# Optimization experiments

Measured on AMD Instinct MI355X. Metric: run time of the kernel, lower is better.

## Reference

```python
import jax, jax.numpy as jnp
import numpy as np
import math

H = 16
D_MODEL = 1024
D_K = 64
BS = 8
SEQ = 1024


def setup_inputs() -> dict:
    key = jax.random.key(0)
    ks = jax.random.split(key, 13)
    s = 1.0 / math.sqrt(D_MODEL)
    inp = {
        "q": jax.random.normal(ks[0], (BS, SEQ, D_MODEL), dtype=jnp.float32),
        "k": jax.random.normal(ks[1], (BS, SEQ, D_MODEL), dtype=jnp.float32),
        "v": jax.random.normal(ks[2], (BS, SEQ, D_MODEL), dtype=jnp.float32),
        "mask": jax.random.randint(ks[3], (BS, SEQ, SEQ), 0, 2, dtype=jnp.int32),
        "Wq": jax.random.normal(ks[4], (D_MODEL, D_MODEL), dtype=jnp.float32) * s,
        "bq": jax.random.normal(ks[5], (D_MODEL,), dtype=jnp.float32) * s,
        "Wk": jax.random.normal(ks[6], (D_MODEL, D_MODEL), dtype=jnp.float32) * s,
        "bk": jax.random.normal(ks[7], (D_MODEL,), dtype=jnp.float32) * s,
        "Wv": jax.random.normal(ks[8], (D_MODEL, D_MODEL), dtype=jnp.float32) * s,
        "bv": jax.random.normal(ks[9], (D_MODEL,), dtype=jnp.float32) * s,
        "Wo": jax.random.normal(ks[10], (D_MODEL, D_MODEL), dtype=jnp.float32) * s,
        "bo": jax.random.normal(ks[11], (D_MODEL,), dtype=jnp.float32) * s,
    }
    return inp


def reference(q, k, v, mask, Wq, bq, Wk, bk, Wv, bv, Wo, bo):
    bs, seq, _ = q.shape
    # projections, split heads: [b, h, s, dk]
    def proj(x, W, b):
        y = x @ W + b
        return y.reshape(bs, seq, H, D_K).transpose(0, 2, 1, 3)
    qh = proj(q, Wq, bq)
    kh = proj(k, Wk, bk)
    vh = proj(v, Wv, bv)
    # scaled dot-product attention (dropout is identity in eval mode)
    scores = jnp.einsum("bhqd,bhkd->bhqk", qh, kh) / math.sqrt(D_K)
    scores = jnp.where(mask[:, None, :, :] == 0, jnp.float32(-1e9), scores)
    attn = jax.nn.softmax(scores, axis=-1)
    ctx = jnp.einsum("bhqk,bhkd->bhqd", attn, vh)
    concat = ctx.transpose(0, 2, 1, 3).reshape(bs, seq, D_MODEL)
    return concat @ Wo + bo
```

## Files before the change

### kernel.cpp

```cpp
#include <hip/hip_runtime.h>
#include <hip/hip_bf16.h>
#include <math.h>

#define HN 16
#define DM 1024
#define DK 64
#define BSZ 8
#define SEQL 1024

typedef __attribute__((ext_vector_type(8))) short bf16x8;
typedef __attribute__((ext_vector_type(4))) short short4v;
typedef __attribute__((ext_vector_type(4))) float f32x4;

__device__ __forceinline__ short f2bf(float f) {
    union { float f; unsigned u; } x; x.f = f;
    unsigned u = x.u + 0x7FFFu + ((x.u >> 16) & 1u);
    return (short)(u >> 16);
}

__global__ __launch_bounds__(256) void transpose_cast(const float* __restrict__ W,
                                                      short* __restrict__ Wt) {
    __shared__ float tile[32][33];
    const int t = threadIdx.x;
    const int k0 = blockIdx.x * 32, n0 = blockIdx.y * 32;
    const int c = t & 31, r = t >> 5;
    #pragma unroll
    for (int p = 0; p < 4; ++p)
        tile[r + 8 * p][c] = W[(size_t)(k0 + r + 8 * p) * DM + n0 + c];
    __syncthreads();
    #pragma unroll
    for (int p = 0; p < 4; ++p)
        Wt[(size_t)(n0 + r + 8 * p) * DM + k0 + c] = f2bf(tile[c][r + 8 * p]);
}

template <int MODE>
__global__ __launch_bounds__(256) void gemm_mfma(const void* __restrict__ Ap,
                                                 const short* __restrict__ Wt,
                                                 const float* __restrict__ bias,
                                                 void* __restrict__ Cp) {
    __shared__ __attribute__((aligned(16))) short As[128][40];
    __shared__ __attribute__((aligned(16))) short Bs[128][40];
    const int t = threadIdx.x;
    const int lane = t & 63, wv = t >> 6;
    const int wm = (wv >> 1) * 64, wn = (wv & 1) * 64;
    const int quad = lane >> 4, l15 = lane & 15;
    const int tileM = blockIdx.x * 128, tileN = blockIdx.y * 128;
    const size_t zoff = (size_t)blockIdx.z * DM * SEQL;

    f32x4 acc[4][4];
    #pragma unroll
    for (int i = 0; i < 4; ++i)
        #pragma unroll
        for (int j = 0; j < 4; ++j) acc[i][j] = {0.f, 0.f, 0.f, 0.f};

    for (int k0 = 0; k0 < DM; k0 += 32) {
        if (MODE == 0) {
            const float* A = (const float*)Ap + zoff;
            const int r0 = t >> 3, c4 = (t & 7) * 4;
            #pragma unroll
            for (int p = 0; p < 4; ++p) {
                int row = r0 + 32 * p;
                float4 v = *(const float4*)(A + (size_t)(tileM + row) * DM + k0 + c4);
                short4v s4 = {f2bf(v.x), f2bf(v.y), f2bf(v.z), f2bf(v.w)};
                *(short4v*)&As[row][c4] = s4;
            }
        } else {
            const short* A = (const short*)Ap + zoff;
            const int r0 = t >> 2, c8 = (t & 3) * 8;
            #pragma unroll
            for (int p = 0; p < 2; ++p) {
                int row = r0 + 64 * p;
                *(bf16x8*)&As[row][c8] =
                    *(const bf16x8*)(A + (size_t)(tileM + row) * DM + k0 + c8);
            }
        }
        {
            const int r0 = t >> 2, c8 = (t & 3) * 8;
            #pragma unroll
            for (int p = 0; p < 2; ++p) {
                int row = r0 + 64 * p;
                *(bf16x8*)&Bs[row][c8] =
                    *(const bf16x8*)(Wt + (size_t)(tileN + row) * DM + k0 + c8);
            }
        }
        __syncthreads();
        bf16x8 a[4], b[4];
        #pragma unroll
        for (int i = 0; i < 4; ++i) a[i] = *(const bf16x8*)&As[wm + i * 16 + l15][quad * 8];
        #pragma unroll
        for (int j = 0; j < 4; ++j) b[j] = *(const bf16x8*)&Bs[wn + j * 16 + l15][quad * 8];
        #pragma unroll
        for (int i = 0; i < 4; ++i)
            #pragma unroll
            for (int j = 0; j < 4; ++j)
                acc[i][j] = __builtin_amdgcn_mfma_f32_16x16x32_bf16(a[i], b[j], acc[i][j], 0, 0, 0);
        __syncthreads();
    }

    #pragma unroll
    for (int i = 0; i < 4; ++i)
        #pragma unroll
        for (int j = 0; j < 4; ++j)
            #pragma unroll
            for (int rr = 0; rr < 4; ++rr) {
                int row = tileM + wm + i * 16 + quad * 4 + rr;
                int col = tileN + wn + j * 16 + l15;
                float v = acc[i][j][rr] + bias[col];
                if (MODE == 0) {
                    short* C = (short*)Cp + zoff;
                    C[((size_t)(col >> 6) * SEQL + row) * DK + (col & 63)] = f2bf(v);
                } else {
                    float* C = (float*)Cp + zoff;
                    C[(size_t)row * DM + col] = v;
                }
            }
}

__global__ __launch_bounds__(256) void attn_mfma(const short* __restrict__ Qw,
                                                 const short* __restrict__ Kw,
                                                 const short* __restrict__ Vw,
                                                 const int* __restrict__ mask,
                                                 short* __restrict__ ctx) {
    __shared__ __attribute__((aligned(16))) short Qs[64][72];
    __shared__ __attribute__((aligned(16))) short Ks[64][72];
    __shared__ __attribute__((aligned(16))) short Vs[64][72];
    __shared__ __attribute__((aligned(16))) short Ps[4][16][72];
    const int t = threadIdx.x;
    const int lane = t & 63, w = t >> 6;
    const int quad = lane >> 4, l15 = lane & 15;
    const int q0 = blockIdx.x * 64;
    const int h = blockIdx.y;
    const size_t zoff = (size_t)blockIdx.z * DM * SEQL;
    const short* Qb = Qw + zoff + (size_t)h * SEQL * DK;
    const short* Kb = Kw + zoff + (size_t)h * SEQL * DK;
    const short* Vb = Vw + zoff + (size_t)h * SEQL * DK;
    const int* mb = mask + (size_t)blockIdx.z * SEQL * SEQL;

    #pragma unroll
    for (int p = 0; p < 2; ++p) {
        int cc = t + 256 * p;
        int row = cc >> 3, off = (cc & 7) * 8;
        *(bf16x8*)&Qs[row][off] = *(const bf16x8*)(Qb + (size_t)(q0 + row) * DK + off);
    }

    f32x4 o[4];
    #pragma unroll
    for (int td = 0; td < 4; ++td) o[td] = {0.f, 0.f, 0.f, 0.f};
    float Lacc[4] = {0.f, 0.f, 0.f, 0.f};

    for (int j0 = 0; j0 < SEQL; j0 += 64) {
        #pragma unroll
        for (int p = 0; p < 2; ++p) {
            int cc = t + 256 * p;
            int row = cc >> 3, off = (cc & 7) * 8;
            *(bf16x8*)&Ks[row][off] = *(const bf16x8*)(Kb + (size_t)(j0 + row) * DK + off);
        }
        {
            int r = t >> 2, c16 = (t & 3) * 16;
            bf16x8 v0 = *(const bf16x8*)(Vb + (size_t)(j0 + r) * DK + c16);
            bf16x8 v1 = *(const bf16x8*)(Vb + (size_t)(j0 + r) * DK + c16 + 8);
            #pragma unroll
            for (int u = 0; u < 8; ++u) Vs[c16 + u][r] = v0[u];
            #pragma unroll
            for (int u = 0; u < 8; ++u) Vs[c16 + 8 + u][r] = v1[u];
        }
        __syncthreads();

        #pragma unroll
        for (int tn = 0; tn < 4; ++tn) {
            f32x4 s = {0.f, 0.f, 0.f, 0.f};
            #pragma unroll
            for (int ks = 0; ks < 2; ++ks) {
                bf16x8 aq = *(const bf16x8*)&Qs[w * 16 + l15][ks * 32 + quad * 8];
                bf16x8 bk = *(const bf16x8*)&Ks[tn * 16 + l15][ks * 32 + quad * 8];
                s = __builtin_amdgcn_mfma_f32_16x16x32_bf16(aq, bk, s, 0, 0, 0);
            }
            #pragma unroll
            for (int rr = 0; rr < 4; ++rr) {
                int rq = q0 + w * 16 + quad * 4 + rr;
                int cj = j0 + tn * 16 + l15;
                float p = mb[(size_t)rq * SEQL + cj] ? __expf(s[rr] * 0.125f) : 0.0f;
                Lacc[rr] += p;
                Ps[w][quad * 4 + rr][tn * 16 + l15] = f2bf(p);
            }
        }
        __syncthreads();

        #pragma unroll
        for (int td = 0; td < 4; ++td)
            #pragma unroll
            for (int ks = 0; ks < 2; ++ks) {
                bf16x8 ap = *(const bf16x8*)&Ps[w][l15][ks * 32 + quad * 8];
                bf16x8 bv = *(const bf16x8*)&Vs[td * 16 + l15][ks * 32 + quad * 8];
                o[td] = __builtin_amdgcn_mfma_f32_16x16x32_bf16(ap, bv, o[td], 0, 0, 0);
            }
        __syncthreads();
    }

    #pragma unroll
    for (int rr = 0; rr < 4; ++rr) {
        float l = Lacc[rr];
        l += __shfl_xor(l, 1);
        l += __shfl_xor(l, 2);
        l += __shfl_xor(l, 4);
        l += __shfl_xor(l, 8);
        Lacc[rr] = 1.0f / l;
    }
    short* cb = ctx + zoff;
    #pragma unroll
    for (int td = 0; td < 4; ++td)
        #pragma unroll
        for (int rr = 0; rr < 4; ++rr) {
            int rq = q0 + w * 16 + quad * 4 + rr;
            int cd = h * 64 + td * 16 + l15;
            cb[(size_t)rq * DM + cd] = f2bf(o[td][rr] * Lacc[rr]);
        }
}

extern "C" void kernel_launch(void* const* d_in, const int* in_sizes, int n_in,
                              void* d_out, int out_size, void* d_ws, size_t ws_size,
                              hipStream_t stream) {
    const float* q  = (const float*)d_in[0];
    const float* k  = (const float*)d_in[1];
    const float* v  = (const float*)d_in[2];
    const int* mask = (const int*)d_in[3];
    const float* Wq = (const float*)d_in[4];
    const float* bq = (const float*)d_in[5];
    const float* Wk = (const float*)d_in[6];
    const float* bk = (const float*)d_in[7];
    const float* Wv = (const float*)d_in[8];
    const float* bv = (const float*)d_in[9];
    const float* Wo = (const float*)d_in[10];
    const float* bo = (const float*)d_in[11];
    float* out = (float*)d_out;

    const size_t MEL = (size_t)1024 * 1024;
    short* wsb = (short*)d_ws;
    short* Wqt = wsb;
    short* Wkt = wsb + MEL;
    short* Wvt = wsb + 2 * MEL;
    short* Wot = wsb + 3 * MEL;

    transpose_cast<<<dim3(32, 32), 256, 0, stream>>>(Wq, Wqt);
    transpose_cast<<<dim3(32, 32), 256, 0, stream>>>(Wk, Wkt);
    transpose_cast<<<dim3(32, 32), 256, 0, stream>>>(Wv, Wvt);
    transpose_cast<<<dim3(32, 32), 256, 0, stream>>>(Wo, Wot);

    const bool full = ws_size >= ((size_t)80 << 20);
    const int zdim = full ? BSZ : 1;
    const int iters = full ? 1 : BSZ;

    const size_t bufEl = full ? 8 * MEL : MEL;
    short* Qw  = wsb + 4 * MEL;
    short* Kw  = Qw + bufEl;
    short* Vw  = Kw + bufEl;
    short* ctx = Vw + bufEl;

    for (int it = 0; it < iters; ++it) {
        const float* qb = q + (size_t)it * MEL;
        const float* kb = k + (size_t)it * MEL;
        const float* vb = v + (size_t)it * MEL;
        const int* mbp  = mask + (size_t)it * MEL;
        float* ob       = out + (size_t)it * MEL;

        gemm_mfma<0><<<dim3(8, 8, zdim), 256, 0, stream>>>(qb, Wqt, bq, Qw);
        gemm_mfma<0><<<dim3(8, 8, zdim), 256, 0, stream>>>(kb, Wkt, bk, Kw);
        gemm_mfma<0><<<dim3(8, 8, zdim), 256, 0, stream>>>(vb, Wvt, bv, Vw);

        attn_mfma<<<dim3(16, 16, zdim), 256, 0, stream>>>(Qw, Kw, Vw, mbp, ctx);

        gemm_mfma<1><<<dim3(8, 8, zdim), 256, 0, stream>>>(ctx, Wot, bo, ob);
    }
}
```

Baseline: 440.8 us.

## Restructure MHA pipeline: bit-packed mask, fused QKV launch, register-resident attention

```diff
diff --git a/kernel.cpp b/kernel.cpp
--- a/kernel.cpp
+++ b/kernel.cpp
@@ -1,6 +1,5 @@
 #include <hip/hip_runtime.h>
 #include <hip/hip_bf16.h>
-#include <math.h>
 
 #define HN 16
 #define DM 1024
@@ -12,14 +11,23 @@
 typedef __attribute__((ext_vector_type(4))) short short4v;
 typedef __attribute__((ext_vector_type(4))) float f32x4;
 
+#define KSCALE 0.18033688011112042f
+
 __device__ __forceinline__ short f2bf(float f) {
     union { float f; unsigned u; } x; x.f = f;
     unsigned u = x.u + 0x7FFFu + ((x.u >> 16) & 1u);
     return (short)(u >> 16);
 }
 
-__global__ __launch_bounds__(256) void transpose_cast(const float* __restrict__ W,
-                                                      short* __restrict__ Wt) {
+__global__ __launch_bounds__(256) void transpose_cast_all(
+    const float* __restrict__ Wq, const float* __restrict__ Wk,
+    const float* __restrict__ Wv, const float* __restrict__ Wo,
+    short* __restrict__ Wqt, short* __restrict__ Wkt,
+    short* __restrict__ Wvt, short* __restrict__ Wot) {
+    const int z = blockIdx.z;
+    const float* W = (z == 0) ? Wq : (z == 1) ? Wk : (z == 2) ? Wv : Wo;
+    short* Wt = (z == 0) ? Wqt : (z == 1) ? Wkt : (z == 2) ? Wvt : Wot;
+    const float scale = (z == 1) ? KSCALE : 1.0f;
     __shared__ float tile[32][33];
     const int t = threadIdx.x;
     const int k0 = blockIdx.x * 32, n0 = blockIdx.y * 32;
@@ -30,14 +38,31 @@
     __syncthreads();
     #pragma unroll
     for (int p = 0; p < 4; ++p)
-        Wt[(size_t)(n0 + r + 8 * p) * DM + k0 + c] = f2bf(tile[c][r + 8 * p]);
-}
-
-template <int MODE>
-__global__ __launch_bounds__(256) void gemm_mfma(const void* __restrict__ Ap,
-                                                 const short* __restrict__ Wt,
-                                                 const float* __restrict__ bias,
-                                                 void* __restrict__ Cp) {
+        Wt[(size_t)(n0 + r + 8 * p) * DM + k0 + c] = f2bf(tile[c][r + 8 * p] * scale);
+}
+
+__global__ __launch_bounds__(256) void pack_mask(const int* __restrict__ mask,
+                                                 unsigned long long* __restrict__ bits) {
+    size_t i = (size_t)blockIdx.x * 256 + threadIdx.x;
+    unsigned long long b = __ballot(mask[i] != 0);
+    if ((threadIdx.x & 63) == 0) bits[i >> 6] = b;
+}
+
+__global__ __launch_bounds__(256) void gemm_qkv(
+    const float* __restrict__ Aq, const float* __restrict__ Ak,
+    const float* __restrict__ Av,
+    const short* __restrict__ Wqt, const short* __restrict__ Wkt,
+    const short* __restrict__ Wvt,
+    const float* __restrict__ bq, const float* __restrict__ bk,
+    const float* __restrict__ bv,
+    short* __restrict__ Qw, short* __restrict__ Kw, short* __restrict__ Vw) {
+    const int which = blockIdx.z;
+    const float* A = (which == 0) ? Aq : (which == 1) ? Ak : Av;
+    const short* Wt = (which == 0) ? Wqt : (which == 1) ? Wkt : Wvt;
+    const float* bias = (which == 0) ? bq : (which == 1) ? bk : bv;
+    short* C = (which == 0) ? Qw : (which == 1) ? Kw : Vw;
+    const float bsc = (which == 1) ? KSCALE : 1.0f;
+
     __shared__ __attribute__((aligned(16))) short As[128][40];
     __shared__ __attribute__((aligned(16))) short Bs[128][40];
     const int t = threadIdx.x;
@@ -45,7 +70,6 @@
     const int wm = (wv >> 1) * 64, wn = (wv & 1) * 64;
     const int quad = lane >> 4, l15 = lane & 15;
     const int tileM = blockIdx.x * 128, tileN = blockIdx.y * 128;
-    const size_t zoff = (size_t)blockIdx.z * DM * SEQL;
 
     f32x4 acc[4][4];
     #pragma unroll
@@ -54,8 +78,7 @@
         for (int j = 0; j < 4; ++j) acc[i][j] = {0.f, 0.f, 0.f, 0.f};
 
     for (int k0 = 0; k0 < DM; k0 += 32) {
-        if (MODE == 0) {
-            const float* A = (const float*)Ap + zoff;
+        {
             const int r0 = t >> 3, c4 = (t & 7) * 4;
             #pragma unroll
             for (int p = 0; p < 4; ++p) {
@@ -64,15 +87,6 @@
                 short4v s4 = {f2bf(v.x), f2bf(v.y), f2bf(v.z), f2bf(v.w)};
                 *(short4v*)&As[row][c4] = s4;
             }
-        } else {
-            const short* A = (const short*)Ap + zoff;
-            const int r0 = t >> 2, c8 = (t & 3) * 8;
-            #pragma unroll
-            for (int p = 0; p < 2; ++p) {
-                int row = r0 + 64 * p;
-                *(bf16x8*)&As[row][c8] =
-                    *(const bf16x8*)(A + (size_t)(tileM + row) * DM + k0 + c8);
-            }
         }
         {
             const int r0 = t >> 2, c8 = (t & 3) * 8;
@@ -105,116 +119,173 @@
             for (int rr = 0; rr < 4; ++rr) {
                 int row = tileM + wm + i * 16 + quad * 4 + rr;
                 int col = tileN + wn + j * 16 + l15;
-                float v = acc[i][j][rr] + bias[col];
-                if (MODE == 0) {
-                    short* C = (short*)Cp + zoff;
+                float v = acc[i][j][rr] + bias[col] * bsc;
+                if (which < 2)
                     C[((size_t)(col >> 6) * SEQL + row) * DK + (col & 63)] = f2bf(v);
-                } else {
-                    float* C = (float*)Cp + zoff;
-                    C[(size_t)row * DM + col] = v;
-                }
-            }
-}
-
-__global__ __launch_bounds__(256) void attn_mfma(const short* __restrict__ Qw,
-                                                 const short* __restrict__ Kw,
-                                                 const short* __restrict__ Vw,
-                                                 const int* __restrict__ mask,
-                                                 short* __restrict__ ctx) {
-    __shared__ __attribute__((aligned(16))) short Qs[64][72];
-    __shared__ __attribute__((aligned(16))) short Ks[64][72];
-    __shared__ __attribute__((aligned(16))) short Vs[64][72];
-    __shared__ __attribute__((aligned(16))) short Ps[4][16][72];
+                else
+                    C[(size_t)col * SEQL + row] = f2bf(v);
+            }
+}
+
+__global__ __launch_bounds__(256) void gemm_out(const short* __restrict__ A,
+                                                const short* __restrict__ Wt,
+                                                const float* __restrict__ bias,
+                                                float* __restrict__ C) {
+    __shared__ __attribute__((aligned(16))) short As[128][40];
+    __shared__ __attribute__((aligned(16))) short Bs[128][40];
+    const int t = threadIdx.x;
+    const int lane = t & 63, wv = t >> 6;
+    const int wm = (wv >> 1) * 64, wn = (wv & 1) * 64;
+    const int quad = lane >> 4, l15 = lane & 15;
+    const int tileM = blockIdx.x * 128, tileN = blockIdx.y * 128;
+
+    f32x4 acc[4][4];
+    #pragma unroll
+    for (int i = 0; i < 4; ++i)
+        #pragma unroll
+        for (int j = 0; j < 4; ++j) acc[i][j] = {0.f, 0.f, 0.f, 0.f};
+
+    for (int k0 = 0; k0 < DM; k0 += 32) {
+        const int r0 = t >> 2, c8 = (t & 3) * 8;
+        #pragma unroll
+        for (int p = 0; p < 2; ++p) {
+            int row = r0 + 64 * p;
+            *(bf16x8*)&As[row][c8] =
+                *(const bf16x8*)(A + (size_t)(tileM + row) * DM + k0 + c8);
+            *(bf16x8*)&Bs[row][c8] =
+                *(const bf16x8*)(Wt + (size_t)(tileN + row) * DM + k0 + c8);
+        }
+        __syncthreads();
+        bf16x8 a[4], b[4];
+        #pragma unroll
+        for (int i = 0; i < 4; ++i) a[i] = *(const bf16x8*)&As[wm + i * 16 + l15][quad * 8];
+        #pragma unroll
+        for (int j = 0; j < 4; ++j) b[j] = *(const bf16x8*)&Bs[wn + j * 16 + l15][quad * 8];
+        #pragma unroll
+        for (int i = 0; i < 4; ++i)
+            #pragma unroll
+            for (int j = 0; j < 4; ++j)
+                acc[i][j] = __builtin_amdgcn_mfma_f32_16x16x32_bf16(a[i], b[j], acc[i][j], 0, 0, 0);
+        __syncthreads();
+    }
+
+    #pragma unroll
+    for (int i = 0; i < 4; ++i)
+        #pragma unroll
+        for (int j = 0; j < 4; ++j)
+            #pragma unroll
+            for (int rr = 0; rr < 4; ++rr) {
+                int row = tileM + wm + i * 16 + quad * 4 + rr;
+                int col = tileN + wn + j * 16 + l15;
+                C[(size_t)row * DM + col] = acc[i][j][rr] + bias[col];
+            }
+}
+
+__global__ __launch_bounds__(256) void attn_mfma2(
+    const short* __restrict__ Qw, const short* __restrict__ Kw,
+    const short* __restrict__ Vt, const unsigned long long* __restrict__ bits,
+    short* __restrict__ ctx) {
+    __shared__ __attribute__((aligned(16))) short Ps[4][32][72];
+    __shared__ __attribute__((aligned(16))) float Ls[4][32];
     const int t = threadIdx.x;
     const int lane = t & 63, w = t >> 6;
     const int quad = lane >> 4, l15 = lane & 15;
-    const int q0 = blockIdx.x * 64;
     const int h = blockIdx.y;
-    const size_t zoff = (size_t)blockIdx.z * DM * SEQL;
-    const short* Qb = Qw + zoff + (size_t)h * SEQL * DK;
-    const short* Kb = Kw + zoff + (size_t)h * SEQL * DK;
-    const short* Vb = Vw + zoff + (size_t)h * SEQL * DK;
-    const int* mb = mask + (size_t)blockIdx.z * SEQL * SEQL;
-
-    #pragma unroll
-    for (int p = 0; p < 2; ++p) {
-        int cc = t + 256 * p;
-        int row = cc >> 3, off = (cc & 7) * 8;
-        *(bf16x8*)&Qs[row][off] = *(const bf16x8*)(Qb + (size_t)(q0 + row) * DK + off);
-    }
-
-    f32x4 o[4];
-    #pragma unroll
-    for (int td = 0; td < 4; ++td) o[td] = {0.f, 0.f, 0.f, 0.f};
-    float Lacc[4] = {0.f, 0.f, 0.f, 0.f};
+    const int qbase = blockIdx.x * 128 + w * 32;
+    const short* Qb = Qw + (size_t)h * SEQL * DK;
+    const short* Kb = Kw + (size_t)h * SEQL * DK;
+    const short* Vb = Vt + (size_t)h * DK * SEQL;
+
+    bf16x8 qf[2][2];
+    #pragma unroll
+    for (int qn = 0; qn < 2; ++qn)
+        #pragma unroll
+        for (int ks = 0; ks < 2; ++ks)
+            qf[qn][ks] = *(const bf16x8*)(Qb + (size_t)(qbase + qn * 16 + l15) * DK +
+                                          ks * 32 + quad * 8);
+
+    f32x4 oc[2][4];
+    #pragma unroll
+    for (int qm = 0; qm < 2; ++qm)
+        #pragma unroll
+        for (int td = 0; td < 4; ++td) oc[qm][td] = {0.f, 0.f, 0.f, 0.f};
+    float Lacc[2] = {0.f, 0.f};
 
     for (int j0 = 0; j0 < SEQL; j0 += 64) {
-        #pragma unroll
-        for (int p = 0; p < 2; ++p) {
-            int cc = t + 256 * p;
-            int row = cc >> 3, off = (cc & 7) * 8;
-            *(bf16x8*)&Ks[row][off] = *(const bf16x8*)(Kb + (size_t)(j0 + row) * DK + off);
+        bf16x8 kf[4][2];
+        #pragma unroll
+        for (int jm = 0; jm < 4; ++jm)
+            #pragma unroll
+            for (int ks = 0; ks < 2; ++ks)
+                kf[jm][ks] = *(const bf16x8*)(Kb + (size_t)(j0 + jm * 16 + l15) * DK +
+                                              ks * 32 + quad * 8);
+        f32x4 st[4][2];
+        #pragma unroll
+        for (int jm = 0; jm < 4; ++jm)
+            #pragma unroll
+            for (int qn = 0; qn < 2; ++qn) {
+                f32x4 s = {0.f, 0.f, 0.f, 0.f};
+                s = __builtin_amdgcn_mfma_f32_16x16x32_bf16(kf[jm][0], qf[qn][0], s, 0, 0, 0);
+                s = __builtin_amdgcn_mfma_f32_16x16x32_bf16(kf[jm][1], qf[qn][1], s, 0, 0, 0);
+                st[jm][qn] = s;
+            }
+        unsigned long long mw[2];
+        #pragma unroll
+        for (int qn = 0; qn < 2; ++qn)
+            mw[qn] = bits[(size_t)(qbase + qn * 16 + l15) * 16 + (j0 >> 6)];
+
+        #pragma unroll
+        for (int jm = 0; jm < 4; ++jm)
+            #pragma unroll
+            for (int qn = 0; qn < 2; ++qn) {
+                short4v p4;
+                #pragma unroll
+                for (int rr = 0; rr < 4; ++rr) {
+                    bool keep = (mw[qn] >> (jm * 16 + quad * 4 + rr)) & 1ull;
+                    float e = exp2f(keep ? st[jm][qn][rr] : -1e30f);
+                    Lacc[qn] += e;
+                    p4[rr] = f2bf(e);
+                }
+                *(short4v*)&Ps[w][qn * 16 + l15][jm * 16 + quad * 4] = p4;
+            }
+
+        #pragma unroll
+        for (int ks = 0; ks < 2; ++ks) {
+            bf16x8 pf[2];
+            #pragma unroll
+            for (int qm = 0; qm < 2; ++qm)
+                pf[qm] = *(const bf16x8*)&Ps[w][qm * 16 + l15][ks * 32 + quad * 8];
+            #pragma unroll
+            for (int td = 0; td < 4; ++td) {
+                bf16x8 vf = *(const bf16x8*)(Vb + (size_t)(td * 16 + l15) * SEQL + j0 +
+                                             ks * 32 + quad * 8);
+                oc[0][td] = __builtin_amdgcn_mfma_f32_16x16x32_bf16(pf[0], vf, oc[0][td], 0, 0, 0);
+                oc[1][td] = __builtin_amdgcn_mfma_f32_16x16x32_bf16(pf[1], vf, oc[1][td], 0, 0, 0);
+            }
         }
-        {
-            int r = t >> 2, c16 = (t & 3) * 16;
-            bf16x8 v0 = *(const bf16x8*)(Vb + (size_t)(j0 + r) * DK + c16);
-            bf16x8 v1 = *(const bf16x8*)(Vb + (size_t)(j0 + r) * DK + c16 + 8);
-            #pragma unroll
-            for (int u = 0; u < 8; ++u) Vs[c16 + u][r] = v0[u];
-            #pragma unroll
-            for (int u = 0; u < 8; ++u) Vs[c16 + 8 + u][r] = v1[u];
-        }
-        __syncthreads();
-
-        #pragma unroll
-        for (int tn = 0; tn < 4; ++tn) {
-            f32x4 s = {0.f, 0.f, 0.f, 0.f};
-            #pragma unroll
-            for (int ks = 0; ks < 2; ++ks) {
-                bf16x8 aq = *(const bf16x8*)&Qs[w * 16 + l15][ks * 32 + quad * 8];
-                bf16x8 bk = *(const bf16x8*)&Ks[tn * 16 + l15][ks * 32 + quad * 8];
-                s = __builtin_amdgcn_mfma_f32_16x16x32_bf16(aq, bk, s, 0, 0, 0);
-            }
+    }
+
+    #pragma unroll
+    for (int qn = 0; qn < 2; ++qn) {
+        float l = Lacc[qn];
+        l += __shfl_xor(l, 16);
+        l += __shfl_xor(l, 32);
+        Ls[w][qn * 16 + l15] = 1.0f / l;
+    }
+    f32x4 rv[2];
+    #pragma unroll
+    for (int qm = 0; qm < 2; ++qm) rv[qm] = *(f32x4*)&Ls[w][qm * 16 + quad * 4];
+
+    #pragma unroll
+    for (int qm = 0; qm < 2; ++qm)
+        #pragma unroll
+        for (int td = 0; td < 4; ++td)
             #pragma unroll
             for (int rr = 0; rr < 4; ++rr) {
-                int rq = q0 + w * 16 + quad * 4 + rr;
-                int cj = j0 + tn * 16 + l15;
-                float p = mb[(size_t)rq * SEQL + cj] ? __expf(s[rr] * 0.125f) : 0.0f;
-                Lacc[rr] += p;
-                Ps[w][quad * 4 + rr][tn * 16 + l15] = f2bf(p);
-            }
-        }
-        __syncthreads();
-
-        #pragma unroll
-        for (int td = 0; td < 4; ++td)
-            #pragma unroll
-            for (int ks = 0; ks < 2; ++ks) {
-                bf16x8 ap = *(const bf16x8*)&Ps[w][l15][ks * 32 + quad * 8];
-                bf16x8 bv = *(const bf16x8*)&Vs[td * 16 + l15][ks * 32 + quad * 8];
-                o[td] = __builtin_amdgcn_mfma_f32_16x16x32_bf16(ap, bv, o[td], 0, 0, 0);
-            }
-        __syncthreads();
-    }
-
-    #pragma unroll
-    for (int rr = 0; rr < 4; ++rr) {
-        float l = Lacc[rr];
-        l += __shfl_xor(l, 1);
-        l += __shfl_xor(l, 2);
-        l += __shfl_xor(l, 4);
-        l += __shfl_xor(l, 8);
-        Lacc[rr] = 1.0f / l;
-    }
-    short* cb = ctx + zoff;
-    #pragma unroll
-    for (int td = 0; td < 4; ++td)
-        #pragma unroll
-        for (int rr = 0; rr < 4; ++rr) {
-            int rq = q0 + w * 16 + quad * 4 + rr;
-            int cd = h * 64 + td * 16 + l15;
-            cb[(size_t)rq * DM + cd] = f2bf(o[td][rr] * Lacc[rr]);
-        }
+                int rq = qbase + qm * 16 + quad * 4 + rr;
+                int cd = h * 64 + td * 16 + l15;
+                ctx[(size_t)rq * DM + cd] = f2bf(oc[qm][td][rr] * rv[qm][rr]);
+            }
 }
 
 extern "C" void kernel_launch(void* const* d_in, const int* in_sizes, int n_in,
@@ -234,41 +305,32 @@
     const float* bo = (const float*)d_in[11];
     float* out = (float*)d_out;
 
+    const size_t MB = (size_t)1 << 20;
     const size_t MEL = (size_t)1024 * 1024;
-    short* wsb = (short*)d_ws;
-    short* Wqt = wsb;
-    short* Wkt = wsb + MEL;
-    short* Wvt = wsb + 2 * MEL;
-    short* Wot = wsb + 3 * MEL;
-
-    transpose_cast<<<dim3(32, 32), 256, 0, stream>>>(Wq, Wqt);
-    transpose_cast<<<dim3(32, 32), 256, 0, stream>>>(Wk, Wkt);
-    transpose_cast<<<dim3(32, 32), 256, 0, stream>>>(Wv, Wvt);
-    transpose_cast<<<dim3(32, 32), 256, 0, stream>>>(Wo, Wot);
-
-    const bool full = ws_size >= ((size_t)80 << 20);
-    const int zdim = full ? BSZ : 1;
-    const int iters = full ? 1 : BSZ;
-
-    const size_t bufEl = full ? 8 * MEL : MEL;
-    short* Qw  = wsb + 4 * MEL;
-    short* Kw  = Qw + bufEl;
-    short* Vw  = Kw + bufEl;
-    short* ctx = Vw + bufEl;
-
-    for (int it = 0; it < iters; ++it) {
-        const float* qb = q + (size_t)it * MEL;
-        const float* kb = k + (size_t)it * MEL;
-        const float* vb = v + (size_t)it * MEL;
-        const int* mbp  = mask + (size_t)it * MEL;
-        float* ob       = out + (size_t)it * MEL;
-
-        gemm_mfma<0><<<dim3(8, 8, zdim), 256, 0, stream>>>(qb, Wqt, bq, Qw);
-        gemm_mfma<0><<<dim3(8, 8, zdim), 256, 0, stream>>>(kb, Wkt, bk, Kw);
-        gemm_mfma<0><<<dim3(8, 8, zdim), 256, 0, stream>>>(vb, Wvt, bv, Vw);
-
-        attn_mfma<<<dim3(16, 16, zdim), 256, 0, stream>>>(Qw, Kw, Vw, mbp, ctx);
-
-        gemm_mfma<1><<<dim3(8, 8, zdim), 256, 0, stream>>>(ctx, Wot, bo, ob);
-    }
-}
+    char* base = (char*)d_ws;
+
+    short* Wqt = (short*)(base + 0 * 2 * MB);
+    short* Wkt = (short*)(base + 1 * 2 * MB);
+    short* Wvt = (short*)(base + 2 * 2 * MB);
+    short* Wot = (short*)(base + 3 * 2 * MB);
+    short* Qw  = (short*)(base + 8 * MB);
+    short* Kw  = (short*)(base + 10 * MB);
+    short* Vw  = (short*)(base + 12 * MB);
+    short* ctx = (short*)(base + 14 * MB);
+
+    unsigned long long* bits = (unsigned long long*)((char*)d_out + 28 * MB);
+
+    transpose_cast_all<<<dim3(32, 32, 4), 256, 0, stream>>>(Wq, Wk, Wv, Wo,
+                                                            Wqt, Wkt, Wvt, Wot);
+    pack_mask<<<(BSZ * SEQL * SEQL) / 256, 256, 0, stream>>>(mask, bits);
+
+    for (int it = 0; it < BSZ; ++it) {
+        const size_t boff = (size_t)it * MEL;
+        gemm_qkv<<<dim3(8, 8, 3), 256, 0, stream>>>(q + boff, k + boff, v + boff,
+                                                    Wqt, Wkt, Wvt, bq, bk, bv,
+                                                    Qw, Kw, Vw);
+        attn_mfma2<<<dim3(8, HN), 256, 0, stream>>>(Qw, Kw, Vw,
+                                                    bits + (size_t)it * SEQL * 16, ctx);
+        gemm_out<<<dim3(8, 8), 256, 0, stream>>>(ctx, Wot, bo, out + boff);
+    }
+}
```

Result: slower. 1.177 ms (+167.1%).
